# Optimization experiments

Hardware: AMD Instinct MI355X
Metric: run time of the kernel (lower is better)

Reference implementation:

```python
import jax, jax.numpy as jnp
import numpy as np

B, S, D = 2, 2048, 1024
H, DK = 16, 64
NUM_BUCKETS, MAX_DIST = 32, 128
EPS = 1e-6


def _relative_position_bucket(q_len, k_len):
    # T5 bidirectional relative position bucketing.
    ctx = jnp.arange(q_len)[:, None]
    mem = jnp.arange(k_len)[None, :]
    rel = mem - ctx  # [q, k]
    nb = NUM_BUCKETS // 2
    ret = (rel > 0).astype(jnp.int32) * nb
    n = jnp.abs(rel)
    max_exact = nb // 2
    is_small = n < max_exact
    n_safe = jnp.maximum(n, 1).astype(jnp.float32)
    val_large = max_exact + (
        jnp.log(n_safe / max_exact) / np.log(MAX_DIST / max_exact) * (nb - max_exact)
    ).astype(jnp.int32)
    val_large = jnp.minimum(val_large, nb - 1)
    return ret + jnp.where(is_small, n, val_large)  # [q, k] int32


def setup_inputs() -> dict:
    key = jax.random.key(0)
    ks = jax.random.split(key, 7)
    s = 0.02
    return {
        "hidden_states": jax.random.normal(ks[0], (B, S, D), jnp.float32),
        "ln_g": jnp.ones((D,), jnp.float32),
        "ln_b": jnp.zeros((D,), jnp.float32),
        "Wq": jax.random.normal(ks[1], (D, H * DK), jnp.float32) * s,
        "Wk": jax.random.normal(ks[2], (D, H * DK), jnp.float32) * s,
        "Wv": jax.random.normal(ks[3], (D, H * DK), jnp.float32) * s,
        "Wo": jax.random.normal(ks[4], (H * DK, D), jnp.float32) * s,
        "rel_bias": jax.random.normal(ks[5], (NUM_BUCKETS, H), jnp.float32) * s,
    }


def reference(hidden_states, ln_g, ln_b, Wq, Wk, Wv, Wo, rel_bias):
    b, s, d = hidden_states.shape
    # LayerNorm (nn.LayerNorm with affine, biased variance)
    mu = jnp.mean(hidden_states, axis=-1, keepdims=True)
    var = jnp.mean(jnp.square(hidden_states - mu), axis=-1, keepdims=True)
    normed = (hidden_states - mu) * jax.lax.rsqrt(var + EPS) * ln_g + ln_b
    # QKV projections (no bias), split heads
    q = (normed @ Wq).reshape(b, s, H, DK)
    k = (normed @ Wk).reshape(b, s, H, DK)
    v = (normed @ Wv).reshape(b, s, H, DK)
    # T5 attention: NO 1/sqrt(d) scaling; learned relative-position bias added to logits
    scores = jnp.einsum("bqhd,bkhd->bhqk", q, k)
    bucket = _relative_position_bucket(s, s)          # [s, s]
    bias = jnp.transpose(rel_bias[bucket], (2, 0, 1))  # [H, s, s]
    attn = jax.nn.softmax(scores + bias[None], axis=-1)
    ctx = jnp.einsum("bhqk,bkhd->bqhd", attn, v).reshape(b, s, H * DK)
    out = ctx @ Wo
    # residual (dropout is identity in eval)
    return hidden_states + out
```

## Files before the change

### kernel.cpp

```cpp
#include <hip/hip_runtime.h>
#include <hip/hip_bf16.h>
#include <math.h>

typedef __attribute__((__ext_vector_type__(8))) short bf16x8;
typedef __attribute__((__ext_vector_type__(4))) float f32x4;
typedef __attribute__((__ext_vector_type__(16))) float f32x16;
typedef __attribute__((__ext_vector_type__(4))) unsigned int u32x4;

#define B_ 2
#define S_ 2048
#define D_ 1024
#define H_ 16
#define DK_ 64
#define M_ (B_*S_)
#define N3_ 3072
#define BIAS_LEN 4096
#define M0_ 24.0f
#define L2E_ 1.4426950408889634f

__device__ __forceinline__ unsigned int cvtpk(float a, float b){
  unsigned int r;
  asm("v_cvt_pk_bf16_f32 %0, %1, %2" : "=v"(r) : "v"(a), "v"(b));
  return r;
}
__device__ __forceinline__ unsigned short f2bf(float f){
  unsigned int r;
  asm("v_cvt_pk_bf16_f32 %0, %1, %2" : "=v"(r) : "v"(f), "v"(f));
  return (unsigned short)r;
}

__device__ __forceinline__ float fexp2(float x){
#if __has_builtin(__builtin_amdgcn_exp2f)
  return __builtin_amdgcn_exp2f(x);
#else
  return __expf(x * 0.6931471805599453f);
#endif
}

__device__ __forceinline__ f32x4 zero4(){
  f32x4 z; z[0]=0.f; z[1]=0.f; z[2]=0.f; z[3]=0.f; return z;
}

__device__ __forceinline__ f32x4 mfma16(bf16x8 a, bf16x8 b, f32x4 c){
  return __builtin_amdgcn_mfma_f32_16x16x32_bf16(a, b, c, 0, 0, 0);
}
__device__ __forceinline__ f32x16 mfma32(bf16x8 a, bf16x8 b, f32x16 c){
  return __builtin_amdgcn_mfma_f32_32x32x16_bf16(a, b, c, 0, 0, 0);
}

__device__ __forceinline__ void gload16(const void* g, void* l){
  __builtin_amdgcn_global_load_lds(
      (const __attribute__((address_space(1))) void*)g,
      (__attribute__((address_space(3))) void*)l, 16, 0, 0);
}

__global__ __launch_bounds__(256) void transpose_cast_kernel(
    const float* __restrict__ Wq, const float* __restrict__ Wk,
    const float* __restrict__ Wv, const float* __restrict__ Wo,
    unsigned short* __restrict__ Wcat_t, unsigned short* __restrict__ Wo_t)
{
  __shared__ float tile[64][65];
  const int k0 = blockIdx.x * 64;
  const int v0 = blockIdx.y * 64;
  const int sel = v0 >> 10;
  const float* W = (sel==0) ? Wq : (sel==1) ? Wk : (sel==2) ? Wv : Wo;
  const int nn0 = v0 & 1023;
  #pragma unroll
  for (int i=0;i<16;i++){
    int idx = i*256 + threadIdx.x;
    int r = idx >> 6, c = idx & 63;
    tile[r][c] = W[(size_t)(k0+r)*1024 + nn0 + c];
  }
  __syncthreads();
  #pragma unroll
  for (int i=0;i<16;i++){
    int idx = i*256 + threadIdx.x;
    int nr = idx >> 6, kc = idx & 63;
    unsigned short bv = f2bf(tile[kc][nr]);
    if (sel < 3) Wcat_t[(size_t)(v0+nr)*1024 + k0 + kc] = bv;
    else         Wo_t[(size_t)(v0-3072+nr)*1024 + k0 + kc] = bv;
  }
}

__global__ __launch_bounds__(256) void bias_tab_kernel(
    const float* __restrict__ rel_bias, float* __restrict__ biasTab)
{
  int t = blockIdx.x*256 + threadIdx.x;
  if (t >= H_*BIAS_LEN) return;
  int h = t / BIAS_LEN;
  int idx = t - h*BIAS_LEN;
  int rel = idx - (S_-1);
  int ret = (rel > 0) ? 16 : 0;
  int n = (rel < 0) ? -rel : rel;
  int bidx;
  if (n < 8) bidx = n;
  else {
    float vl = logf((float)n * 0.125f) / 2.7725887f * 8.0f;
    int v = 8 + (int)vl;
    bidx = (v < 15) ? v : 15;
  }
  biasTab[t] = (rel_bias[(ret + bidx)*H_ + h] - M0_) * L2E_;
}

__global__ __launch_bounds__(256) void ln_kernel(
    const float* __restrict__ x, const float* __restrict__ g,
    const float* __restrict__ bta, unsigned short* __restrict__ out)
{
  const int row = blockIdx.x;
  const int tid = threadIdx.x;
  float4 v = ((const float4*)(x + (size_t)row*D_))[tid];
  float s  = v.x+v.y+v.z+v.w;
  float ss = v.x*v.x+v.y*v.y+v.z*v.z+v.w*v.w;
  #pragma unroll
  for (int off=1; off<64; off<<=1){ s += __shfl_xor(s,off,64); ss += __shfl_xor(ss,off,64); }
  __shared__ float rs[4], rss[4];
  const int wid = tid >> 6, lane = tid & 63;
  if (lane == 0){ rs[wid] = s; rss[wid] = ss; }
  __syncthreads();
  s  = rs[0]+rs[1]+rs[2]+rs[3];
  ss = rss[0]+rss[1]+rss[2]+rss[3];
  float mu  = s * (1.0f/1024.0f);
  float var = ss * (1.0f/1024.0f) - mu*mu;
  float rstd = rsqrtf(var + 1e-6f);
  float4 gg = ((const float4*)g)[tid];
  float4 bb = ((const float4*)bta)[tid];
  uint2 o;
  o.x = cvtpk((v.x-mu)*rstd*gg.x + bb.x, (v.y-mu)*rstd*gg.y + bb.y);
  o.y = cvtpk((v.z-mu)*rstd*gg.z + bb.z, (v.w-mu)*rstd*gg.w + bb.w);
  ((uint2*)(out + (size_t)row*D_))[tid] = o;
}

template<int MODE>
__global__ __launch_bounds__(256) void gemm_kernel(
    const unsigned short* __restrict__ A,
    const unsigned short* __restrict__ Bt,
    const float* __restrict__ resid,
    unsigned short* __restrict__ Qb,
    unsigned short* __restrict__ Kb,
    unsigned short* __restrict__ Vtb,
    float* __restrict__ outf,
    int Ndim, int Kdim)
{
  __shared__ unsigned short As[128*64];
  __shared__ unsigned short Bs[128*64];
  const int tid = threadIdx.x;
  const int wid = tid >> 6, lane = tid & 63;
  const int lr = lane & 15, lg = lane >> 4;
  const int wm = (wid >> 1) * 64, wn = (wid & 1) * 64;

  const int nbx = gridDim.x;
  const int total = nbx * gridDim.y;
  const int flat = blockIdx.y * nbx + blockIdx.x;
  const int swz = (flat & 7) * (total >> 3) + (flat >> 3);
  const int m0 = (swz % nbx) * 128, n0 = (swz / nbx) * 128;

  f32x4 acc[4][4];
  #pragma unroll
  for (int i=0;i<4;i++)
    #pragma unroll
    for (int j=0;j<4;j++) acc[i][j] = zero4();

  for (int k0 = 0; k0 < Kdim; k0 += 64) {
    __syncthreads();
    #pragma unroll
    for (int i=0;i<4;i++){
      int c = i*256 + tid;
      int row = c >> 3, ch = c & 7;
      int chs = ch ^ (row & 7);
      gload16(A  + (size_t)(m0+row)*Kdim + k0 + chs*8, As + c*8);
      gload16(Bt + (size_t)(n0+row)*Kdim + k0 + chs*8, Bs + c*8);
    }
    __syncthreads();
    #pragma unroll
    for (int kk=0;kk<2;kk++){
      bf16x8 aF[4], bF[4];
      #pragma unroll
      for (int mi=0;mi<4;mi++){
        int row = wm + mi*16 + lr;
        aF[mi] = *(const bf16x8*)&As[row*64 + (((kk*4+lg) ^ (row & 7)) * 8)];
      }
      #pragma unroll
      for (int ni=0;ni<4;ni++){
        int row = wn + ni*16 + lr;
        bF[ni] = *(const bf16x8*)&Bs[row*64 + (((kk*4+lg) ^ (row & 7)) * 8)];
      }
      #pragma unroll
      for (int mi=0;mi<4;mi++)
        #pragma unroll
        for (int ni=0;ni<4;ni++)
          acc[mi][ni] = mfma16(aF[mi], bF[ni], acc[mi][ni]);
    }
  }

  if (MODE == 1) {
    #pragma unroll
    for (int mi=0;mi<4;mi++)
      #pragma unroll
      for (int ni=0;ni<4;ni++)
        #pragma unroll
        for (int r=0;r<4;r++){
          int m = m0 + wm + mi*16 + lg*4 + r;
          int n = n0 + wn + ni*16 + lr;
          outf[(size_t)m*Ndim + n] = acc[mi][ni][r] + resid[(size_t)m*Ndim + n];
        }
  } else {
    const int seln = n0 >> 10;
    if (seln == 2) {
      #pragma unroll
      for (int mi=0;mi<4;mi++)
        #pragma unroll
        for (int ni=0;ni<4;ni++){
          int m = m0 + wm + mi*16 + lg*4;
          int n = n0 + wn + ni*16 + lr;
          int nn = n & 1023, hh = nn >> 6, dk = nn & 63;
          int b = m >> 11, s = m & 2047;
          uint2 u;
          u.x = cvtpk(acc[mi][ni][0], acc[mi][ni][1]);
          u.y = cvtpk(acc[mi][ni][2], acc[mi][ni][3]);
          *(uint2*)(Vtb + (((size_t)(b*H_+hh))*DK_ + dk)*S_ + s) = u;
        }
    } else {
      unsigned short* __restrict__ dst = (seln == 0) ? Qb : Kb;
      #pragma unroll
      for (int mi=0;mi<4;mi++)
        #pragma unroll
        for (int ni=0;ni<4;ni++)
          #pragma unroll
          for (int r=0;r<4;r++){
            int m = m0 + wm + mi*16 + lg*4 + r;
            int n = n0 + wn + ni*16 + lr;
            int nn = n & 1023, hh = nn >> 6, dk = nn & 63;
            int b = m >> 11, s = m & 2047;
            dst[(((size_t)(b*H_+hh))*S_ + s)*DK_ + dk] = f2bf(acc[mi][ni][r]);
          }
    }
  }
}

__global__ __launch_bounds__(256, 2) void attn_kernel(
    const unsigned short* __restrict__ Qb,
    const unsigned short* __restrict__ Kb,
    const unsigned short* __restrict__ Vtb,
    const float* __restrict__ biasTab,
    const float* __restrict__ rel_bias,
    unsigned short* __restrict__ ctxb)
{
  __shared__ unsigned short Ks[64*64];
  __shared__ unsigned short Vts[64*64];
  __shared__ float biasW[2176];
  __shared__ float lshare[4][32];

  const int tid = threadIdx.x;
  const int wid = tid >> 6, lane = tid & 63;
  const int ql = lane & 31;
  const int hi = lane >> 5;
  const int bh = blockIdx.y;
  const int h = bh & (H_-1);
  const int b = bh >> 4;
  const int q0blk = blockIdx.x * 128;
  const int q0w = q0blk + wid*32;
  const int qlocal = wid*32 + ql;

  const int wb = 1920 - q0blk;
  for (int i = tid; i < 2176; i += 256) biasW[i] = biasTab[(size_t)h*BIAS_LEN + wb + i];

  const float cpos = (rel_bias[31*H_ + h] - M0_) * L2E_;
  const float cneg = (rel_bias[15*H_ + h] - M0_) * L2E_;

  const unsigned short* Qp = Qb + ((size_t)bh*S_ + q0w + ql)*DK_;
  bf16x8 qf[4];
  #pragma unroll
  for (int c=0;c<4;c++) qf[c] = *(const bf16x8*)(Qp + 16*c + 8*hi);

  const unsigned short* Ksrc = Kb  + (size_t)bh*S_*DK_;
  const unsigned short* Vsrc = Vtb + (size_t)bh*DK_*S_;
  const int c0 = tid, c1 = tid + 256;
  const int r0 = c0 >> 3, ch0 = c0 & 7;
  const int r1 = c1 >> 3, ch1 = c1 & 7;

  f32x16 acc[2];
  #pragma unroll
  for (int i=0;i<16;i++){ acc[0][i]=0.f; acc[1][i]=0.f; }
  float lsum = 0.f;

  bf16x8 sk0 = *(const bf16x8*)(Ksrc + (size_t)(0 + r0)*DK_ + ch0*8);
  bf16x8 sk1 = *(const bf16x8*)(Ksrc + (size_t)(0 + r1)*DK_ + ch1*8);
  bf16x8 sv0 = *(const bf16x8*)(Vsrc + (size_t)r0*S_ + 0 + ch0*8);
  bf16x8 sv1 = *(const bf16x8*)(Vsrc + (size_t)r1*S_ + 0 + ch1*8);

  for (int k0 = 0; k0 < S_; k0 += 64) {
    __syncthreads();
    *(bf16x8*)&Ks [r0*64 + ((ch0 ^ (r0&7))*8)] = sk0;
    *(bf16x8*)&Ks [r1*64 + ((ch1 ^ (r1&7))*8)] = sk1;
    *(bf16x8*)&Vts[r0*64 + ((ch0 ^ (r0&7))*8)] = sv0;
    *(bf16x8*)&Vts[r1*64 + ((ch1 ^ (r1&7))*8)] = sv1;
    __syncthreads();
    if (k0 + 64 < S_) {
      int kn = k0 + 64;
      sk0 = *(const bf16x8*)(Ksrc + (size_t)(kn + r0)*DK_ + ch0*8);
      sk1 = *(const bf16x8*)(Ksrc + (size_t)(kn + r1)*DK_ + ch1*8);
      sv0 = *(const bf16x8*)(Vsrc + (size_t)r0*S_ + kn + ch0*8);
      sv1 = *(const bf16x8*)(Vsrc + (size_t)r1*S_ + kn + ch1*8);
    }

    const bool uni_pos = (k0 >= q0w + 122);
    const bool uni_neg = (k0 + 63 <= q0w - 91);

    unsigned int W0[2][4], W1[2][4], O0[2][4], O1[2][4];

    #pragma unroll
    for (int st=0; st<2; ++st){
      f32x16 s;
      #pragma unroll
      for (int i=0;i<16;i++) s[i]=0.f;
      const int arow = st*32 + ql;
      #pragma unroll
      for (int c=0;c<4;c++){
        bf16x8 kf = *(const bf16x8*)&Ks[arow*64 + (((hi + 2*c) ^ (arow&7))*8)];
        s = mfma32(kf, qf[c], s);
      }
      float p[16];
      if (uni_pos) {
        #pragma unroll
        for (int r=0;r<16;r++) p[r] = fexp2(__builtin_fmaf(s[r], L2E_, cpos));
      } else if (uni_neg) {
        #pragma unroll
        for (int r=0;r<16;r++) p[r] = fexp2(__builtin_fmaf(s[r], L2E_, cneg));
      } else {
        #pragma unroll
        for (int r=0;r<16;r++){
          int key = k0 + st*32 + (r&3) + 8*(r>>2) + 4*hi;
          p[r] = fexp2(__builtin_fmaf(s[r], L2E_, biasW[key - qlocal + 127]));
        }
      }
      #pragma unroll
      for (int r=0;r<16;r++) lsum += p[r];
      #pragma unroll
      for (int m=0;m<4;m++){
        W0[st][m] = cvtpk(p[4*m+0], p[4*m+1]);
        W1[st][m] = cvtpk(p[4*m+2], p[4*m+3]);
        O0[st][m] = __shfl_xor(W0[st][m], 32);
        O1[st][m] = __shfl_xor(W1[st][m], 32);
      }
    }

    #pragma unroll
    for (int st=0; st<2; ++st){
      #pragma unroll
      for (int c=0;c<2;c++){
        unsigned int a0 = hi ? O0[st][2*c+1] : W0[st][2*c+0];
        unsigned int a1 = hi ? O1[st][2*c+1] : W1[st][2*c+0];
        unsigned int a2 = hi ? W0[st][2*c+1] : O0[st][2*c+0];
        unsigned int a3 = hi ? W1[st][2*c+1] : O1[st][2*c+0];
        u32x4 pu; pu[0]=a0; pu[1]=a1; pu[2]=a2; pu[3]=a3;
        bf16x8 pav = __builtin_bit_cast(bf16x8, pu);
        const int vch = 4*st + 2*c + hi;
        #pragma unroll
        for (int dt=0; dt<2; ++dt){
          const int vrow = ql + 32*dt;
          bf16x8 vf = *(const bf16x8*)&Vts[vrow*64 + ((vch ^ (vrow&7))*8)];
          acc[dt] = mfma32(pav, vf, acc[dt]);
        }
      }
    }
  }

  float ltot = lsum + __shfl_xor(lsum, 32);
  lshare[wid][ql] = 1.0f / ltot;
  __syncthreads();
  #pragma unroll
  for (int r=0;r<16;r++){
    const int qr = (r&3) + 8*(r>>2) + 4*hi;
    const float li = lshare[wid][qr];
    const int q = q0w + qr;
    #pragma unroll
    for (int dt=0; dt<2; ++dt){
      const int d = ql + 32*dt;
      ctxb[((size_t)(b*S_ + q))*(H_*DK_) + h*DK_ + d] = f2bf(acc[dt][r] * li);
    }
  }
}

extern "C" void kernel_launch(void* const* d_in, const int* in_sizes, int n_in,
                              void* d_out, int out_size, void* d_ws, size_t ws_size,
                              hipStream_t stream) {
  const float* hidden   = (const float*)d_in[0];
  const float* ln_g     = (const float*)d_in[1];
  const float* ln_b     = (const float*)d_in[2];
  const float* Wq       = (const float*)d_in[3];
  const float* Wk       = (const float*)d_in[4];
  const float* Wv       = (const float*)d_in[5];
  const float* Wo       = (const float*)d_in[6];
  const float* rel_bias = (const float*)d_in[7];
  float* out = (float*)d_out;

  char* ws = (char*)d_ws;
  const size_t off_ln   = 0;
  const size_t off_wcat = 8388608;
  const size_t off_wo   = 14680064;
  const size_t off_q    = 16777216;
  const size_t off_k    = 25165824;
  const size_t off_vt   = 33554432;
  const size_t off_ctx  = 41943040;
  const size_t off_bias = 50331648;

  unsigned short* ln_out  = (unsigned short*)(ws + off_ln);
  unsigned short* Wcat_t  = (unsigned short*)(ws + off_wcat);
  unsigned short* Wo_t    = (unsigned short*)(ws + off_wo);
  unsigned short* Qb      = (unsigned short*)(ws + off_q);
  unsigned short* Kb      = (unsigned short*)(ws + off_k);
  unsigned short* Vtb     = (unsigned short*)(ws + off_vt);
  unsigned short* ctxb    = (unsigned short*)(ws + off_ctx);
  float*          biasTab = (float*)(ws + off_bias);

  transpose_cast_kernel<<<dim3(16,64), 256, 0, stream>>>(Wq, Wk, Wv, Wo, Wcat_t, Wo_t);
  bias_tab_kernel<<<(H_*BIAS_LEN + 255)/256, 256, 0, stream>>>(rel_bias, biasTab);
  ln_kernel<<<M_, 256, 0, stream>>>(hidden, ln_g, ln_b, ln_out);
  gemm_kernel<0><<<dim3(M_/128, N3_/128), 256, 0, stream>>>(
      ln_out, Wcat_t, nullptr, Qb, Kb, Vtb, nullptr, N3_, D_);
  attn_kernel<<<dim3(S_/128, B_*H_), 256, 0, stream>>>(Qb, Kb, Vtb, biasTab, rel_bias, ctxb);
  gemm_kernel<1><<<dim3(M_/128, D_/128), 256, 0, stream>>>(
      ctxb, Wo_t, hidden, nullptr, nullptr, nullptr, out, D_, D_);
}
```

Before: 139.5 us.

## Split attention over two key halves with a combine kernel

Splits the key dimension of the attention kernel into two halves via a third grid dimension, so twice as many blocks run. Each half writes unnormalized partial outputs and row sums, which a new combine kernel adds and normalizes. The change also drops the LDS bias window in favour of direct global bias reads, swaps the XOR swizzle for a padded LDS stride, and raises launch bounds to 4 blocks per CU. In exchange it adds partial-output traffic, an extra launch, and bf16 rounding of the partial results. The fixed max offset (M0) makes the merge a plain sum.

```diff
diff --git a/kernel.cpp b/kernel.cpp
--- a/kernel.cpp
+++ b/kernel.cpp
@@ -17,6 +17,7 @@
 #define BIAS_LEN 4096
 #define M0_ 24.0f
 #define L2E_ 1.4426950408889634f
+#define KSTRIDE 66
 
 __device__ __forceinline__ unsigned int cvtpk(float a, float b){
   unsigned int r;
@@ -27,6 +28,9 @@
   unsigned int r;
   asm("v_cvt_pk_bf16_f32 %0, %1, %2" : "=v"(r) : "v"(f), "v"(f));
   return (unsigned short)r;
+}
+__device__ __forceinline__ float bf2f(unsigned short u){
+  union{unsigned int i; float f;} v; v.i = ((unsigned int)u)<<16; return v.f;
 }
 
 __device__ __forceinline__ float fexp2(float x){
@@ -237,18 +241,17 @@
   }
 }
 
-__global__ __launch_bounds__(256, 2) void attn_kernel(
+__global__ __launch_bounds__(256, 4) void attn_kernel(
     const unsigned short* __restrict__ Qb,
     const unsigned short* __restrict__ Kb,
     const unsigned short* __restrict__ Vtb,
     const float* __restrict__ biasTab,
     const float* __restrict__ rel_bias,
-    unsigned short* __restrict__ ctxb)
-{
-  __shared__ unsigned short Ks[64*64];
-  __shared__ unsigned short Vts[64*64];
-  __shared__ float biasW[2176];
-  __shared__ float lshare[4][32];
+    unsigned short* __restrict__ Opart,
+    float* __restrict__ Lpart)
+{
+  __shared__ unsigned short Ks[64*KSTRIDE];
+  __shared__ unsigned short Vts[64*KSTRIDE];
 
   const int tid = threadIdx.x;
   const int wid = tid >> 6, lane = tid & 63;
@@ -257,15 +260,14 @@
   const int bh = blockIdx.y;
   const int h = bh & (H_-1);
   const int b = bh >> 4;
+  const int kg = blockIdx.z;
+  const int kbase = kg << 10;
   const int q0blk = blockIdx.x * 128;
   const int q0w = q0blk + wid*32;
-  const int qlocal = wid*32 + ql;
-
-  const int wb = 1920 - q0blk;
-  for (int i = tid; i < 2176; i += 256) biasW[i] = biasTab[(size_t)h*BIAS_LEN + wb + i];
 
   const float cpos = (rel_bias[31*H_ + h] - M0_) * L2E_;
   const float cneg = (rel_bias[15*H_ + h] - M0_) * L2E_;
+  const float* bG = biasTab + (size_t)h*BIAS_LEN + 2047 - (q0w + ql);
 
   const unsigned short* Qp = Qb + ((size_t)bh*S_ + q0w + ql)*DK_;
   bf16x8 qf[4];
@@ -283,19 +285,19 @@
   for (int i=0;i<16;i++){ acc[0][i]=0.f; acc[1][i]=0.f; }
   float lsum = 0.f;
 
-  bf16x8 sk0 = *(const bf16x8*)(Ksrc + (size_t)(0 + r0)*DK_ + ch0*8);
-  bf16x8 sk1 = *(const bf16x8*)(Ksrc + (size_t)(0 + r1)*DK_ + ch1*8);
-  bf16x8 sv0 = *(const bf16x8*)(Vsrc + (size_t)r0*S_ + 0 + ch0*8);
-  bf16x8 sv1 = *(const bf16x8*)(Vsrc + (size_t)r1*S_ + 0 + ch1*8);
-
-  for (int k0 = 0; k0 < S_; k0 += 64) {
+  bf16x8 sk0 = *(const bf16x8*)(Ksrc + (size_t)(kbase + r0)*DK_ + ch0*8);
+  bf16x8 sk1 = *(const bf16x8*)(Ksrc + (size_t)(kbase + r1)*DK_ + ch1*8);
+  bf16x8 sv0 = *(const bf16x8*)(Vsrc + (size_t)r0*S_ + kbase + ch0*8);
+  bf16x8 sv1 = *(const bf16x8*)(Vsrc + (size_t)r1*S_ + kbase + ch1*8);
+
+  for (int k0 = kbase; k0 < kbase + 1024; k0 += 64) {
     __syncthreads();
-    *(bf16x8*)&Ks [r0*64 + ((ch0 ^ (r0&7))*8)] = sk0;
-    *(bf16x8*)&Ks [r1*64 + ((ch1 ^ (r1&7))*8)] = sk1;
-    *(bf16x8*)&Vts[r0*64 + ((ch0 ^ (r0&7))*8)] = sv0;
-    *(bf16x8*)&Vts[r1*64 + ((ch1 ^ (r1&7))*8)] = sv1;
+    *(bf16x8*)&Ks [r0*KSTRIDE + ch0*8] = sk0;
+    *(bf16x8*)&Ks [r1*KSTRIDE + ch1*8] = sk1;
+    *(bf16x8*)&Vts[r0*KSTRIDE + ch0*8] = sv0;
+    *(bf16x8*)&Vts[r1*KSTRIDE + ch1*8] = sv1;
     __syncthreads();
-    if (k0 + 64 < S_) {
+    if (k0 + 64 < kbase + 1024) {
       int kn = k0 + 64;
       sk0 = *(const bf16x8*)(Ksrc + (size_t)(kn + r0)*DK_ + ch0*8);
       sk1 = *(const bf16x8*)(Ksrc + (size_t)(kn + r1)*DK_ + ch1*8);
@@ -316,7 +318,7 @@
       const int arow = st*32 + ql;
       #pragma unroll
       for (int c=0;c<4;c++){
-        bf16x8 kf = *(const bf16x8*)&Ks[arow*64 + (((hi + 2*c) ^ (arow&7))*8)];
+        bf16x8 kf = *(const bf16x8*)&Ks[arow*KSTRIDE + (2*c+hi)*8];
         s = mfma32(kf, qf[c], s);
       }
       float p[16];
@@ -330,7 +332,7 @@
         #pragma unroll
         for (int r=0;r<16;r++){
           int key = k0 + st*32 + (r&3) + 8*(r>>2) + 4*hi;
-          p[r] = fexp2(__builtin_fmaf(s[r], L2E_, biasW[key - qlocal + 127]));
+          p[r] = fexp2(__builtin_fmaf(s[r], L2E_, bG[key]));
         }
       }
       #pragma unroll
@@ -358,7 +360,7 @@
         #pragma unroll
         for (int dt=0; dt<2; ++dt){
           const int vrow = ql + 32*dt;
-          bf16x8 vf = *(const bf16x8*)&Vts[vrow*64 + ((vch ^ (vrow&7))*8)];
+          bf16x8 vf = *(const bf16x8*)&Vts[vrow*KSTRIDE + vch*8];
           acc[dt] = mfma32(pav, vf, acc[dt]);
         }
       }
@@ -366,19 +368,42 @@
   }
 
   float ltot = lsum + __shfl_xor(lsum, 32);
-  lshare[wid][ql] = 1.0f / ltot;
-  __syncthreads();
+  if (hi == 0) Lpart[((size_t)kg*B_*H_ + bh)*S_ + q0w + ql] = ltot;
   #pragma unroll
   for (int r=0;r<16;r++){
     const int qr = (r&3) + 8*(r>>2) + 4*hi;
-    const float li = lshare[wid][qr];
     const int q = q0w + qr;
     #pragma unroll
     for (int dt=0; dt<2; ++dt){
       const int d = ql + 32*dt;
-      ctxb[((size_t)(b*S_ + q))*(H_*DK_) + h*DK_ + d] = f2bf(acc[dt][r] * li);
-    }
-  }
+      Opart[(size_t)kg*M_*D_ + ((size_t)(b*S_ + q)*H_ + h)*DK_ + d] = f2bf(acc[dt][r]);
+    }
+  }
+}
+
+__global__ __launch_bounds__(256) void combine_kernel(
+    const unsigned short* __restrict__ Opart, const float* __restrict__ Lpart,
+    unsigned short* __restrict__ ctxb)
+{
+  const int t = blockIdx.x*256 + threadIdx.x;
+  const int f = t*8;
+  const int qgl = f >> 10;
+  const int h = (f >> 6) & 15;
+  const int bh = (qgl >> 11)*H_ + h;
+  const int s = qgl & 2047;
+  const float l0 = Lpart[(size_t)bh*S_ + s];
+  const float l1 = Lpart[(size_t)B_*H_*S_ + (size_t)bh*S_ + s];
+  const float linv = 1.0f / (l0 + l1);
+  bf16x8 p0 = *(const bf16x8*)(Opart + f);
+  bf16x8 p1 = *(const bf16x8*)(Opart + (size_t)M_*D_ + f);
+  u32x4 o;
+  #pragma unroll
+  for (int j=0;j<4;j++){
+    float a = (bf2f((unsigned short)p0[2*j+0]) + bf2f((unsigned short)p1[2*j+0])) * linv;
+    float c = (bf2f((unsigned short)p0[2*j+1]) + bf2f((unsigned short)p1[2*j+1])) * linv;
+    o[j] = cvtpk(a, c);
+  }
+  *(u32x4*)(ctxb + f) = o;
 }
 
 extern "C" void kernel_launch(void* const* d_in, const int* in_sizes, int n_in,
@@ -397,12 +422,13 @@
   char* ws = (char*)d_ws;
   const size_t off_ln   = 0;
   const size_t off_wcat = 8388608;
-  const size_t off_wo   = 14680064;
   const size_t off_q    = 16777216;
   const size_t off_k    = 25165824;
   const size_t off_vt   = 33554432;
   const size_t off_ctx  = 41943040;
   const size_t off_bias = 50331648;
+  const size_t off_lp   = 50593792;
+  const size_t off_wo   = 51118080;
 
   unsigned short* ln_out  = (unsigned short*)(ws + off_ln);
   unsigned short* Wcat_t  = (unsigned short*)(ws + off_wcat);
@@ -412,13 +438,17 @@
   unsigned short* Vtb     = (unsigned short*)(ws + off_vt);
   unsigned short* ctxb    = (unsigned short*)(ws + off_ctx);
   float*          biasTab = (float*)(ws + off_bias);
+  float*          Lpart   = (float*)(ws + off_lp);
+  unsigned short* Opart   = (unsigned short*)(ws + 0);
 
   transpose_cast_kernel<<<dim3(16,64), 256, 0, stream>>>(Wq, Wk, Wv, Wo, Wcat_t, Wo_t);
   bias_tab_kernel<<<(H_*BIAS_LEN + 255)/256, 256, 0, stream>>>(rel_bias, biasTab);
   ln_kernel<<<M_, 256, 0, stream>>>(hidden, ln_g, ln_b, ln_out);
   gemm_kernel<0><<<dim3(M_/128, N3_/128), 256, 0, stream>>>(
       ln_out, Wcat_t, nullptr, Qb, Kb, Vtb, nullptr, N3_, D_);
-  attn_kernel<<<dim3(S_/128, B_*H_), 256, 0, stream>>>(Qb, Kb, Vtb, biasTab, rel_bias, ctxb);
+  attn_kernel<<<dim3(S_/128, B_*H_, 2), 256, 0, stream>>>(
+      Qb, Kb, Vtb, biasTab, rel_bias, Opart, Lpart);
+  combine_kernel<<<(M_*D_/8)/256, 256, 0, stream>>>(Opart, Lpart, ctxb);
   gemm_kernel<1><<<dim3(M_/128, D_/128), 256, 0, stream>>>(
       ctxb, Wo_t, hidden, nullptr, nullptr, nullptr, out, D_, D_);
 }
```

After: 194.6 us. 1.4x slower.
